# Kernel optimization log

Hardware: AMD Instinct MI355X
Metric: run time of the kernel (lower is better)

Reference implementation:

```python
import jax, jax.numpy as jnp
import numpy as np

B, N, CIN, H, OUT, L, K = 8, 512, 64, 64, 64, 256, 3
EPS = 1e-5


def setup_inputs() -> dict:
    key = jax.random.key(0)
    ks = jax.random.split(key, 12)
    def unif(k, shape, fan):
        s = 1.0 / np.sqrt(fan)
        return jax.random.uniform(k, shape, jnp.float32, -s, s)
    return {
        "x": jax.random.normal(ks[0], (B, N, CIN, L), jnp.float32),
        "adj": jax.random.uniform(ks[1], (B, N, N), jnp.float32),
        # temp_conv1: Conv1d(CIN->H, k=3)
        "w1": unif(ks[2], (H, CIN, K), CIN * K),
        "b1": unif(ks[3], (H,), CIN * K),
        # graph_conv: Linear-style (H,H) + bias, stdv=1/sqrt(out_features)
        "gw": unif(ks[4], (H, H), H),
        "gb": unif(ks[5], (H,), H),
        # temp_conv2: Conv1d(H->OUT, k=3)
        "w2": unif(ks[6], (OUT, H, K), H * K),
        "b2": unif(ks[7], (OUT,), H * K),
        # residual: Conv1d(CIN->OUT, k=1) == pointwise linear
        "wr": unif(ks[8], (OUT, CIN), CIN),
        "br": unif(ks[9], (OUT,), CIN),
        # BatchNorm2d(OUT) affine params
        "gamma": jnp.ones((OUT,), jnp.float32),
        "beta": jnp.zeros((OUT,), jnp.float32),
    }


def _conv1d(x, w, b, pad):
    # x: (B, N, C, L) -> flatten node dim into batch, NCH conv
    b_, n_, c, l = x.shape
    y = jax.lax.conv_general_dilated(
        x.reshape(b_ * n_, c, l), w, window_strides=(1,),
        padding=[(pad, pad)], dimension_numbers=("NCH", "OIH", "NCH"))
    y = y + b[None, :, None]
    return y.reshape(b_, n_, w.shape[0], l)


def reference(x, adj, w1, b1, gw, gb, w2, b2, wr, br, gamma, beta):
    pad = (K - 1) // 2
    # residual branch: 1x1 conv over channels
    residual = jnp.einsum("bncl,oc->bnol", x, wr) + br[None, None, :, None]
    # temporal conv 1
    out = _conv1d(x, w1, b1, pad)                      # (B,N,H,L)
    # graph conv over all timesteps at once (replaces per-t Python loop)
    xw = jnp.einsum("bnhl,hd->bndl", out, gw)          # (B,N,H,L)
    out = jnp.einsum("bnm,bmdl->bndl", adj, xw) + gb[None, None, :, None]
    # temporal conv 2
    out = _conv1d(out, w2, b2, pad)                    # (B,N,OUT,L)
    out = out + residual
    # BatchNorm2d over channel axis (training-mode batch stats, biased var)
    mean = jnp.mean(out, axis=(0, 1, 3), keepdims=True)
    var = jnp.mean(jnp.square(out - mean), axis=(0, 1, 3), keepdims=True)
    out = (out - mean) * jax.lax.rsqrt(var + EPS)
    out = out * gamma[None, None, :, None] + beta[None, None, :, None]
    return jax.nn.relu(out)
```

## Files before the change

kernel.cpp:

```cpp
#include <hip/hip_runtime.h>
#include <hip/hip_bf16.h>
#include <stdint.h>


typedef unsigned short u16;
typedef unsigned int   u32;
typedef __attribute__((ext_vector_type(8))) short           bf16x8;
typedef __attribute__((ext_vector_type(8))) unsigned short  u16x8;
typedef __attribute__((ext_vector_type(4))) unsigned short  u16x4;
typedef __attribute__((ext_vector_type(4))) float           f32x4;

__device__ __forceinline__ float bf2f(u16 v){
  union { u32 u; float f; } x; x.u = ((u32)v) << 16; return x.f;
}
__device__ __forceinline__ u16 f2bf(float f){
  __hip_bfloat16 h = __float2bfloat16(f);
  return *reinterpret_cast<u16*>(&h);
}
__device__ __forceinline__ u32 swz(int row, int cbyte){
  return (u32)(row * 128) + (u32)(cbyte ^ ((row & 7) << 4));
}

__device__ __forceinline__ void stage_Tf(const float* __restrict__ src, u16* dst, int t){
  const int c0 = (t & 31) * 2;
  const int l0 = (t >> 5) * 32;
  #pragma unroll
  for (int v = 0; v < 8; ++v){
    f32x4 a = *(const f32x4*)(src + (size_t)c0 * 256 + l0 + v * 4);
    f32x4 b = *(const f32x4*)(src + (size_t)(c0 + 1) * 256 + l0 + v * 4);
    #pragma unroll
    for (int e = 0; e < 4; ++e){
      u32 p = (u32)f2bf(a[e]) | ((u32)f2bf(b[e]) << 16);
      *(u32*)((char*)dst + swz(l0 + v * 4 + e, c0 * 2)) = p;
    }
  }
}
__device__ __forceinline__ void stage_Tb(const u16* __restrict__ src, u16* dst, int t){
  const int c0 = (t & 31) * 2;
  const int l0 = (t >> 5) * 32;
  #pragma unroll
  for (int v = 0; v < 4; ++v){
    u16x8 a = *(const u16x8*)(src + (size_t)c0 * 256 + l0 + v * 8);
    u16x8 b = *(const u16x8*)(src + (size_t)(c0 + 1) * 256 + l0 + v * 8);
    #pragma unroll
    for (int e = 0; e < 8; ++e){
      u32 p = (u32)a[e] | ((u32)b[e] << 16);
      *(u32*)((char*)dst + swz(l0 + v * 8 + e, c0 * 2)) = p;
    }
  }
}

__global__ __launch_bounds__(256) void k_prep(const float* __restrict__ w1, const float* __restrict__ gw,
    const float* __restrict__ w2, const float* __restrict__ wr,
    u16* __restrict__ w1t, u16* __restrict__ gwt, u16* __restrict__ w2t, u16* __restrict__ wrt){
  int t = threadIdx.x;
  for (int e = t; e < 12288; e += 256){
    int tap = e >> 12, rem = e & 4095, o = rem >> 6, c = rem & 63;
    w1t[e] = f2bf(w1[(o * 64 + c) * 3 + tap]);
    w2t[e] = f2bf(w2[(o * 64 + c) * 3 + tap]);
  }
  for (int e = t; e < 4096; e += 256){
    int d = e >> 6, h = e & 63;
    gwt[e] = f2bf(gw[h * 64 + d]);
    wrt[e] = f2bf(wr[e]);
  }
}

__global__ __launch_bounds__(256) void k_p1(const float* __restrict__ x,
    const u16* __restrict__ w1t, const float* __restrict__ b1v,
    const u16* __restrict__ gwt, u16* __restrict__ outA){
  __shared__ u16 tile[16384];
  const int t = threadIdx.x;
  const size_t bn = (size_t)blockIdx.x + (size_t)blockIdx.y * 512;
  stage_Tf(x + bn * 16384, tile, t);
  __syncthreads();
  const int w = t >> 6, ln = t & 63, lq = ln >> 4, lr = ln & 15;
  const bf16x8 z8 = {};
  f32x4 acc[4][4];
  #pragma unroll
  for (int i = 0; i < 4; ++i)
    #pragma unroll
    for (int j = 0; j < 4; ++j) acc[i][j] = (f32x4){0.f, 0.f, 0.f, 0.f};

  #pragma unroll
  for (int tap = 0; tap < 3; ++tap){
    #pragma unroll
    for (int kk = 0; kk < 2; ++kk){
      bf16x8 A[4];
      #pragma unroll
      for (int fo = 0; fo < 4; ++fo)
        A[fo] = *(const bf16x8*)(w1t + tap * 4096 + (fo * 16 + lr) * 64 + kk * 32 + lq * 8);
      #pragma unroll
      for (int fc = 0; fc < 4; ++fc){
        int r = w * 64 + fc * 16 + lr + tap - 1;
        int rc = r < 0 ? 0 : (r > 255 ? 255 : r);
        bf16x8 B = *(const bf16x8*)((char*)tile + swz(rc, kk * 64 + lq * 16));
        if (r != rc) B = z8;
        #pragma unroll
        for (int fo = 0; fo < 4; ++fo)
          acc[fo][fc] = __builtin_amdgcn_mfma_f32_16x16x32_bf16(A[fo], B, acc[fo][fc], 0, 0, 0);
      }
    }
  }
  __syncthreads();
  #pragma unroll
  for (int fo = 0; fo < 4; ++fo){
    float b0 = b1v[fo * 16 + lq * 4 + 0];
    float b1_ = b1v[fo * 16 + lq * 4 + 1];
    float b2_ = b1v[fo * 16 + lq * 4 + 2];
    float b3 = b1v[fo * 16 + lq * 4 + 3];
    #pragma unroll
    for (int fc = 0; fc < 4; ++fc){
      int l = w * 64 + fc * 16 + lr;
      u32 p0 = (u32)f2bf(acc[fo][fc][0] + b0) | ((u32)f2bf(acc[fo][fc][1] + b1_) << 16);
      u32 p1 = (u32)f2bf(acc[fo][fc][2] + b2_) | ((u32)f2bf(acc[fo][fc][3] + b3) << 16);
      char* p = (char*)tile + swz(l, fo * 32 + lq * 8);
      *(u32*)p = p0;
      *(u32*)(p + 4) = p1;
    }
  }
  f32x4 acc2[4][4];
  #pragma unroll
  for (int i = 0; i < 4; ++i)
    #pragma unroll
    for (int j = 0; j < 4; ++j) acc2[i][j] = (f32x4){0.f, 0.f, 0.f, 0.f};
  #pragma unroll
  for (int kk = 0; kk < 2; ++kk){
    bf16x8 A[4];
    #pragma unroll
    for (int fo = 0; fo < 4; ++fo)
      A[fo] = *(const bf16x8*)(gwt + (fo * 16 + lr) * 64 + kk * 32 + lq * 8);
    #pragma unroll
    for (int fc = 0; fc < 4; ++fc){
      int l = w * 64 + fc * 16 + lr;
      bf16x8 B = *(const bf16x8*)((char*)tile + swz(l, kk * 64 + lq * 16));
      #pragma unroll
      for (int fo = 0; fo < 4; ++fo)
        acc2[fo][fc] = __builtin_amdgcn_mfma_f32_16x16x32_bf16(A[fo], B, acc2[fo][fc], 0, 0, 0);
    }
  }
  u16* op = outA + bn * 16384;
  #pragma unroll
  for (int fo = 0; fo < 4; ++fo)
    #pragma unroll
    for (int fc = 0; fc < 4; ++fc){
      int l = w * 64 + fc * 16 + lr;
      #pragma unroll
      for (int r2 = 0; r2 < 4; ++r2)
        op[(fo * 16 + lq * 4 + r2) * 256 + l] = f2bf(acc2[fo][fc][r2]);
    }
}

__global__ __launch_bounds__(256) void k_p3(const u16* __restrict__ xw,
    const float* __restrict__ adj, const float* __restrict__ gbv, u16* __restrict__ outB){
  __shared__ u16 At[8192];
  __shared__ u16 Bt[8192];
  const int t = threadIdx.x;
  const int jt = blockIdx.x, nt = blockIdx.y, b = blockIdx.z;
  const float* adjb = adj + ((size_t)b * 512 + (size_t)nt * 128) * 512;
  const u16* Xb = xw + (size_t)b * 8388608 + (size_t)jt * 128;
  const int w = t >> 6, ln = t & 63, lq = ln >> 4, lr = ln & 15;
  const int wrow = w >> 1, wcol = w & 1;
  const int mpair = t & 31, jq = t >> 5;
  f32x4 acc[4][4];
  #pragma unroll
  for (int i = 0; i < 4; ++i)
    #pragma unroll
    for (int j = 0; j < 4; ++j) acc[i][j] = (f32x4){0.f, 0.f, 0.f, 0.f};

  for (int ks = 0; ks < 8; ++ks){
    #pragma unroll
    for (int it = 0; it < 8; ++it){
      int c = it * 256 + t;
      int row = c >> 4, mc = c & 15;
      f32x4 v = *(const f32x4*)(adjb + (size_t)row * 512 + ks * 64 + mc * 4);
      u16x4 pk;
      #pragma unroll
      for (int e = 0; e < 4; ++e) pk[e] = f2bf(v[e]);
      *(u16x4*)((char*)At + (u32)(row * 128) + (u32)((mc * 8) ^ ((row & 7) << 4))) = pk;
    }
    {
      const u16* s0 = Xb + (size_t)(ks * 64 + mpair * 2) * 16384 + jq * 16;
      const u16* s1 = s0 + 16384;
      #pragma unroll
      for (int v2 = 0; v2 < 2; ++v2){
        u16x8 a = *(const u16x8*)(s0 + v2 * 8);
        u16x8 bb = *(const u16x8*)(s1 + v2 * 8);
        #pragma unroll
        for (int e = 0; e < 8; ++e){
          u32 p = (u32)a[e] | ((u32)bb[e] << 16);
          *(u32*)((char*)Bt + swz(jq * 16 + v2 * 8 + e, mpair * 4)) = p;
        }
      }
    }
    __syncthreads();
    #pragma unroll
    for (int kk = 0; kk < 2; ++kk){
      bf16x8 Af[4], Bf[4];
      #pragma unroll
      for (int f = 0; f < 4; ++f){
        int ra = wrow * 64 + f * 16 + lr;
        Af[f] = *(const bf16x8*)((char*)At + swz(ra, kk * 64 + lq * 16));
        int rb = wcol * 64 + f * 16 + lr;
        Bf[f] = *(const bf16x8*)((char*)Bt + swz(rb, kk * 64 + lq * 16));
      }
      #pragma unroll
      for (int fr = 0; fr < 4; ++fr)
        #pragma unroll
        for (int fc = 0; fc < 4; ++fc)
          acc[fr][fc] = __builtin_amdgcn_mfma_f32_16x16x32_bf16(Af[fr], Bf[fc], acc[fr][fc], 0, 0, 0);
    }
    __syncthreads();
  }
  const float gb = gbv[jt >> 1];
  u16* ob = outB + ((size_t)b * 512 + (size_t)nt * 128) * 16384 + (size_t)jt * 128;
  #pragma unroll
  for (int fr = 0; fr < 4; ++fr)
    #pragma unroll
    for (int fc = 0; fc < 4; ++fc)
      #pragma unroll
      for (int r2 = 0; r2 < 4; ++r2){
        int n_ = wrow * 64 + fr * 16 + lq * 4 + r2;
        int j_ = wcol * 64 + fc * 16 + lr;
        ob[(size_t)n_ * 16384 + j_] = f2bf(acc[fr][fc][r2] + gb);
      }
}

__global__ __launch_bounds__(256) void k_p4(const u16* __restrict__ g,
    const float* __restrict__ x, const u16* __restrict__ w2t, const float* __restrict__ b2v,
    const u16* __restrict__ wrt, const float* __restrict__ brv,
    u16* __restrict__ outP, float* __restrict__ spart){
  __shared__ u16 gt[16384];
  __shared__ u16 xt[16384];
  const int t = threadIdx.x;
  const size_t bn = (size_t)blockIdx.x + (size_t)blockIdx.y * 512;
  stage_Tb(g + bn * 16384, gt, t);
  stage_Tf(x + bn * 16384, xt, t);
  __syncthreads();
  const int w = t >> 6, ln = t & 63, lq = ln >> 4, lr = ln & 15;
  const bf16x8 z8 = {};
  f32x4 acc[4][4];
  #pragma unroll
  for (int i = 0; i < 4; ++i)
    #pragma unroll
    for (int j = 0; j < 4; ++j) acc[i][j] = (f32x4){0.f, 0.f, 0.f, 0.f};

  #pragma unroll
  for (int tap = 0; tap < 3; ++tap){
    #pragma unroll
    for (int kk = 0; kk < 2; ++kk){
      bf16x8 A[4];
      #pragma unroll
      for (int fo = 0; fo < 4; ++fo)
        A[fo] = *(const bf16x8*)(w2t + tap * 4096 + (fo * 16 + lr) * 64 + kk * 32 + lq * 8);
      #pragma unroll
      for (int fc = 0; fc < 4; ++fc){
        int r = w * 64 + fc * 16 + lr + tap - 1;
        int rc = r < 0 ? 0 : (r > 255 ? 255 : r);
        bf16x8 B = *(const bf16x8*)((char*)gt + swz(rc, kk * 64 + lq * 16));
        if (r != rc) B = z8;
        #pragma unroll
        for (int fo = 0; fo < 4; ++fo)
          acc[fo][fc] = __builtin_amdgcn_mfma_f32_16x16x32_bf16(A[fo], B, acc[fo][fc], 0, 0, 0);
      }
    }
  }
  #pragma unroll
  for (int kk = 0; kk < 2; ++kk){
    bf16x8 A[4];
    #pragma unroll
    for (int fo = 0; fo < 4; ++fo)
      A[fo] = *(const bf16x8*)(wrt + (fo * 16 + lr) * 64 + kk * 32 + lq * 8);
    #pragma unroll
    for (int fc = 0; fc < 4; ++fc){
      int l = w * 64 + fc * 16 + lr;
      bf16x8 B = *(const bf16x8*)((char*)xt + swz(l, kk * 64 + lq * 16));
      #pragma unroll
      for (int fo = 0; fo < 4; ++fo)
        acc[fo][fc] = __builtin_amdgcn_mfma_f32_16x16x32_bf16(A[fo], B, acc[fo][fc], 0, 0, 0);
    }
  }
  float psum[16], psq[16];
  #pragma unroll
  for (int i = 0; i < 16; ++i){ psum[i] = 0.f; psq[i] = 0.f; }
  u16* op = outP + bn * 16384;
  #pragma unroll
  for (int fo = 0; fo < 4; ++fo){
    float bb[4];
    #pragma unroll
    for (int r2 = 0; r2 < 4; ++r2){
      int o = fo * 16 + lq * 4 + r2;
      bb[r2] = b2v[o] + brv[o];
    }
    #pragma unroll
    for (int fc = 0; fc < 4; ++fc){
      int l = w * 64 + fc * 16 + lr;
      #pragma unroll
      for (int r2 = 0; r2 < 4; ++r2){
        float v = acc[fo][fc][r2] + bb[r2];
        op[(fo * 16 + lq * 4 + r2) * 256 + l] = f2bf(v);
        psum[fo * 4 + r2] += v;
        psq[fo * 4 + r2] += v * v;
      }
    }
  }
  #pragma unroll
  for (int i = 0; i < 16; ++i){
    #pragma unroll
    for (int m = 1; m < 16; m <<= 1){
      psum[i] += __shfl_xor(psum[i], m, 64);
      psq[i]  += __shfl_xor(psq[i],  m, 64);
    }
  }
  __syncthreads();
  float* sc = (float*)gt;
  if (lr == 0){
    #pragma unroll
    for (int i = 0; i < 16; ++i){
      int o = (i >> 2) * 16 + lq * 4 + (i & 3);
      sc[w * 128 + o]      = psum[i];
      sc[w * 128 + 64 + o] = psq[i];
    }
  }
  __syncthreads();
  if (t < 128){
    float tot = sc[t] + sc[128 + t] + sc[256 + t] + sc[384 + t];
    spart[(size_t)t * 4096 + bn] = tot;
  }
}

__global__ __launch_bounds__(256) void k_p5(const float* __restrict__ part, float* __restrict__ fin){
  const int o = blockIdx.x, t = threadIdx.x;
  float s1 = 0.f, s2 = 0.f;
  for (int k = t; k < 4096; k += 256){
    s1 += part[(size_t)o * 4096 + k];
    s2 += part[(size_t)(64 + o) * 4096 + k];
  }
  #pragma unroll
  for (int m = 32; m; m >>= 1){
    s1 += __shfl_down(s1, m, 64);
    s2 += __shfl_down(s2, m, 64);
  }
  __shared__ float red[8];
  if ((t & 63) == 0){ red[(t >> 6) * 2] = s1; red[(t >> 6) * 2 + 1] = s2; }
  __syncthreads();
  if (t == 0){
    float S1 = red[0] + red[2] + red[4] + red[6];
    float S2 = red[1] + red[3] + red[5] + red[7];
    const float invN = 1.f / 1048576.f;
    float mean = S1 * invN;
    float var = S2 * invN - mean * mean;
    fin[o] = mean;
    fin[64 + o] = rsqrtf(var + 1e-5f);
  }
}

__global__ __launch_bounds__(256) void k_p6(const u16* __restrict__ pre, const float* __restrict__ fin,
    const float* __restrict__ gamma, const float* __restrict__ beta, float* __restrict__ out){
  const size_t nchunk = 8388608;
  for (size_t i = (size_t)blockIdx.x * 256 + threadIdx.x; i < nchunk; i += (size_t)gridDim.x * 256){
    int o = (int)((i >> 5) & 63);
    float sca = fin[64 + o] * gamma[o];
    float off = beta[o] - fin[o] * sca;
    u16x8 v = *(const u16x8*)(pre + i * 8);
    f32x4 o0, o1;
    #pragma unroll
    for (int e = 0; e < 4; ++e){
      float f0 = bf2f(v[e]) * sca + off;
      float f1 = bf2f(v[4 + e]) * sca + off;
      o0[e] = f0 > 0.f ? f0 : 0.f;
      o1[e] = f1 > 0.f ? f1 : 0.f;
    }
    *(f32x4*)(out + i * 8)     = o0;
    *(f32x4*)(out + i * 8 + 4) = o1;
  }
}

extern "C" void kernel_launch(void* const* d_in, const int* in_sizes, int n_in,
                              void* d_out, int out_size, void* d_ws, size_t ws_size,
                              hipStream_t stream){
  const float* x     = (const float*)d_in[0];
  const float* adj   = (const float*)d_in[1];
  const float* w1    = (const float*)d_in[2];
  const float* b1    = (const float*)d_in[3];
  const float* gw    = (const float*)d_in[4];
  const float* gb    = (const float*)d_in[5];
  const float* w2    = (const float*)d_in[6];
  const float* b2    = (const float*)d_in[7];
  const float* wr    = (const float*)d_in[8];
  const float* br    = (const float*)d_in[9];
  const float* gamma = (const float*)d_in[10];
  const float* beta  = (const float*)d_in[11];
  (void)in_sizes; (void)n_in; (void)out_size; (void)ws_size;

  char* ws = (char*)d_ws;
  u16*   bufA  = (u16*)ws;
  float* spart = (float*)(ws + 134217728);
  float* sfin  = (float*)(ws + 136314880);
  u16*   w1t   = (u16*)(ws + 136315392);
  u16*   gwt   = (u16*)(ws + 136339968);
  u16*   w2t   = (u16*)(ws + 136348160);
  u16*   wrt   = (u16*)(ws + 136372736);
  u16*   gbuf  = (u16*)d_out;

  k_prep<<<1, 256, 0, stream>>>(w1, gw, w2, wr, w1t, gwt, w2t, wrt);
  k_p1<<<dim3(512, 8, 1), 256, 0, stream>>>(x, w1t, b1, gwt, bufA);
  k_p3<<<dim3(128, 4, 8), 256, 0, stream>>>(bufA, adj, gb, gbuf);
  k_p4<<<dim3(512, 8, 1), 256, 0, stream>>>(gbuf, x, w2t, b2, wrt, br, bufA, spart);
  k_p5<<<64, 256, 0, stream>>>(spart, sfin);
  k_p6<<<2048, 256, 0, stream>>>(bufA, sfin, gamma, beta, (float*)d_out);
}
```

Measured before the change: 599.9 us.

## Compute residual 1x1 conv in first pass, store bf16, drop x reread

The residual pointwise conv moves from k_p4 into k_p1, which already has x staged in shared memory. The result is stored as bf16 in the second half of the output buffer in a thread-contiguous layout, so k_p4 no longer rereads the fp32 x tensor (64 MB) and reads a 32 MB bf16 residual instead. This halves k_p4's residual read traffic and its shared memory, at the cost of an extra 32 MB write in k_p1 and bf16 rounding of the residual. k_p6 also precomputes per-channel scale and offset into shared memory.

```diff
diff --git a/kernel.cpp b/kernel.cpp
--- a/kernel.cpp
+++ b/kernel.cpp
@@ -68,7 +68,8 @@
 
 __global__ __launch_bounds__(256) void k_p1(const float* __restrict__ x,
     const u16* __restrict__ w1t, const float* __restrict__ b1v,
-    const u16* __restrict__ gwt, u16* __restrict__ outA){
+    const u16* __restrict__ gwt, const u16* __restrict__ wrt,
+    u16* __restrict__ outA, u16* __restrict__ outR){
   __shared__ u16 tile[16384];
   const int t = threadIdx.x;
   const size_t bn = (size_t)blockIdx.x + (size_t)blockIdx.y * 512;
@@ -76,12 +77,49 @@
   __syncthreads();
   const int w = t >> 6, ln = t & 63, lq = ln >> 4, lr = ln & 15;
   const bf16x8 z8 = {};
+
+  {
+    f32x4 racc[4][4];
+    #pragma unroll
+    for (int i = 0; i < 4; ++i)
+      #pragma unroll
+      for (int j = 0; j < 4; ++j) racc[i][j] = (f32x4){0.f, 0.f, 0.f, 0.f};
+    #pragma unroll
+    for (int kk = 0; kk < 2; ++kk){
+      bf16x8 A[4];
+      #pragma unroll
+      for (int fo = 0; fo < 4; ++fo)
+        A[fo] = *(const bf16x8*)(wrt + (fo * 16 + lr) * 64 + kk * 32 + lq * 8);
+      #pragma unroll
+      for (int fc = 0; fc < 4; ++fc){
+        int l = w * 64 + fc * 16 + lr;
+        bf16x8 B = *(const bf16x8*)((char*)tile + swz(l, kk * 64 + lq * 16));
+        #pragma unroll
+        for (int fo = 0; fo < 4; ++fo)
+          racc[fo][fc] = __builtin_amdgcn_mfma_f32_16x16x32_bf16(A[fo], B, racc[fo][fc], 0, 0, 0);
+      }
+    }
+    u16* rp = outR + bn * 16384 + t * 64;
+    #pragma unroll
+    for (int v = 0; v < 8; ++v){
+      u16x8 ov;
+      const int fo = v >> 1;
+      #pragma unroll
+      for (int h = 0; h < 2; ++h){
+        const int fc = (v & 1) * 2 + h;
+        #pragma unroll
+        for (int r2 = 0; r2 < 4; ++r2)
+          ov[h * 4 + r2] = f2bf(racc[fo][fc][r2]);
+      }
+      *(u16x8*)(rp + v * 8) = ov;
+    }
+  }
+
   f32x4 acc[4][4];
   #pragma unroll
   for (int i = 0; i < 4; ++i)
     #pragma unroll
     for (int j = 0; j < 4; ++j) acc[i][j] = (f32x4){0.f, 0.f, 0.f, 0.f};
-
   #pragma unroll
   for (int tap = 0; tap < 3; ++tap){
     #pragma unroll
@@ -227,15 +265,13 @@
 }
 
 __global__ __launch_bounds__(256) void k_p4(const u16* __restrict__ g,
-    const float* __restrict__ x, const u16* __restrict__ w2t, const float* __restrict__ b2v,
-    const u16* __restrict__ wrt, const float* __restrict__ brv,
+    const u16* __restrict__ resv, const u16* __restrict__ w2t,
+    const float* __restrict__ b2v, const float* __restrict__ brv,
     u16* __restrict__ outP, float* __restrict__ spart){
   __shared__ u16 gt[16384];
-  __shared__ u16 xt[16384];
   const int t = threadIdx.x;
   const size_t bn = (size_t)blockIdx.x + (size_t)blockIdx.y * 512;
   stage_Tb(g + bn * 16384, gt, t);
-  stage_Tf(x + bn * 16384, xt, t);
   __syncthreads();
   const int w = t >> 6, ln = t & 63, lq = ln >> 4, lr = ln & 15;
   const bf16x8 z8 = {};
@@ -265,45 +301,41 @@
       }
     }
   }
-  #pragma unroll
-  for (int kk = 0; kk < 2; ++kk){
-    bf16x8 A[4];
-    #pragma unroll
-    for (int fo = 0; fo < 4; ++fo)
-      A[fo] = *(const bf16x8*)(wrt + (fo * 16 + lr) * 64 + kk * 32 + lq * 8);
+
+  float bball[16];
+  #pragma unroll
+  for (int fo = 0; fo < 4; ++fo)
+    #pragma unroll
+    for (int r2 = 0; r2 < 4; ++r2){
+      int o = fo * 16 + lq * 4 + r2;
+      bball[fo * 4 + r2] = b2v[o] + brv[o];
+    }
+  float psum[16], psq[16];
+  #pragma unroll
+  for (int i = 0; i < 16; ++i){ psum[i] = 0.f; psq[i] = 0.f; }
+
+  const u16* rp = resv + bn * 16384 + t * 64;
+  u16x8 rv[8];
+  #pragma unroll
+  for (int v = 0; v < 8; ++v) rv[v] = *(const u16x8*)(rp + v * 8);
+
+  u16* op = outP + bn * 16384;
+  #pragma unroll
+  for (int fo = 0; fo < 4; ++fo){
     #pragma unroll
     for (int fc = 0; fc < 4; ++fc){
       int l = w * 64 + fc * 16 + lr;
-      bf16x8 B = *(const bf16x8*)((char*)xt + swz(l, kk * 64 + lq * 16));
-      #pragma unroll
-      for (int fo = 0; fo < 4; ++fo)
-        acc[fo][fc] = __builtin_amdgcn_mfma_f32_16x16x32_bf16(A[fo], B, acc[fo][fc], 0, 0, 0);
-    }
-  }
-  float psum[16], psq[16];
-  #pragma unroll
-  for (int i = 0; i < 16; ++i){ psum[i] = 0.f; psq[i] = 0.f; }
-  u16* op = outP + bn * 16384;
-  #pragma unroll
-  for (int fo = 0; fo < 4; ++fo){
-    float bb[4];
-    #pragma unroll
-    for (int r2 = 0; r2 < 4; ++r2){
-      int o = fo * 16 + lq * 4 + r2;
-      bb[r2] = b2v[o] + brv[o];
-    }
-    #pragma unroll
-    for (int fc = 0; fc < 4; ++fc){
-      int l = w * 64 + fc * 16 + lr;
       #pragma unroll
       for (int r2 = 0; r2 < 4; ++r2){
-        float v = acc[fo][fc][r2] + bb[r2];
-        op[(fo * 16 + lq * 4 + r2) * 256 + l] = f2bf(v);
-        psum[fo * 4 + r2] += v;
-        psq[fo * 4 + r2] += v * v;
-      }
-    }
-  }
+        float val = acc[fo][fc][r2] + bball[fo * 4 + r2]
+                  + bf2f(rv[fo * 2 + (fc >> 1)][(fc & 1) * 4 + r2]);
+        op[(fo * 16 + lq * 4 + r2) * 256 + l] = f2bf(val);
+        psum[fo * 4 + r2] += val;
+        psq[fo * 4 + r2] += val * val;
+      }
+    }
+  }
+
   #pragma unroll
   for (int i = 0; i < 16; ++i){
     #pragma unroll
@@ -357,22 +389,29 @@
 
 __global__ __launch_bounds__(256) void k_p6(const u16* __restrict__ pre, const float* __restrict__ fin,
     const float* __restrict__ gamma, const float* __restrict__ beta, float* __restrict__ out){
+  __shared__ float ssca[64], soff[64];
+  const int tt = threadIdx.x;
+  if (tt < 64){
+    float sc = fin[64 + tt] * gamma[tt];
+    ssca[tt] = sc;
+    soff[tt] = beta[tt] - fin[tt] * sc;
+  }
+  __syncthreads();
   const size_t nchunk = 8388608;
-  for (size_t i = (size_t)blockIdx.x * 256 + threadIdx.x; i < nchunk; i += (size_t)gridDim.x * 256){
+  for (size_t i = (size_t)blockIdx.x * 256 + tt; i < nchunk; i += (size_t)gridDim.x * 256){
     int o = (int)((i >> 5) & 63);
-    float sca = fin[64 + o] * gamma[o];
-    float off = beta[o] - fin[o] * sca;
+    float sca = ssca[o], off = soff[o];
     u16x8 v = *(const u16x8*)(pre + i * 8);
-    f32x4 o0, o1;
+    f32x4 oa, ob;
     #pragma unroll
     for (int e = 0; e < 4; ++e){
       float f0 = bf2f(v[e]) * sca + off;
       float f1 = bf2f(v[4 + e]) * sca + off;
-      o0[e] = f0 > 0.f ? f0 : 0.f;
-      o1[e] = f1 > 0.f ? f1 : 0.f;
-    }
-    *(f32x4*)(out + i * 8)     = o0;
-    *(f32x4*)(out + i * 8 + 4) = o1;
+      oa[e] = f0 > 0.f ? f0 : 0.f;
+      ob[e] = f1 > 0.f ? f1 : 0.f;
+    }
+    *(f32x4*)(out + i * 8)     = oa;
+    *(f32x4*)(out + i * 8 + 4) = ob;
   }
 }
 
@@ -402,11 +441,12 @@
   u16*   w2t   = (u16*)(ws + 136348160);
   u16*   wrt   = (u16*)(ws + 136372736);
   u16*   gbuf  = (u16*)d_out;
+  u16*   bufR  = (u16*)d_out + 67108864;
 
   k_prep<<<1, 256, 0, stream>>>(w1, gw, w2, wr, w1t, gwt, w2t, wrt);
-  k_p1<<<dim3(512, 8, 1), 256, 0, stream>>>(x, w1t, b1, gwt, bufA);
+  k_p1<<<dim3(512, 8, 1), 256, 0, stream>>>(x, w1t, b1, gwt, wrt, bufA, bufR);
   k_p3<<<dim3(128, 4, 8), 256, 0, stream>>>(bufA, adj, gb, gbuf);
-  k_p4<<<dim3(512, 8, 1), 256, 0, stream>>>(gbuf, x, w2t, b2, wrt, br, bufA, spart);
+  k_p4<<<dim3(512, 8, 1), 256, 0, stream>>>(gbuf, bufR, w2t, b2, br, bufA, spart);
   k_p5<<<64, 256, 0, stream>>>(spart, sfin);
   k_p6<<<2048, 256, 0, stream>>>(bufA, sfin, gamma, beta, (float*)d_out);
 }
```

New measurement: 587.7 us. 1.02x faster.
